# Performance work log

Measured on AMD Instinct MI355X. Metric: run time of the kernel, lower is better.

Reference implementation:

```python
import jax, jax.numpy as jnp
import numpy as np
import math

KEY_SIZE = 128  # init arg; scale = 1/sqrt(key_size)


def setup_inputs() -> dict:
    key = jax.random.key(0)
    kq, kk, kv = jax.random.split(key, 3)
    B, LQ, LK, D, DV = 16, 2048, 2048, 128, 128
    q = jax.random.normal(kq, (B, LQ, D), dtype=jnp.float32)
    k = jax.random.normal(kk, (B, LK, D), dtype=jnp.float32)
    v = jax.random.normal(kv, (B, LK, DV), dtype=jnp.float32)
    return {"q": q, "k": k, "v": v}


def reference(q, k, v):
    scale = 1.0 / math.sqrt(KEY_SIZE)
    # scores: [B, Lq, Lk]
    scores = jnp.einsum('bqd,bkd->bqk', q, k) * scale
    probs = jax.nn.softmax(scores, axis=-1)
    # dropout with p=0.0 is identity (eval-equivalent)
    return jnp.einsum('bqk,bkv->bqv', probs, v)
```

## Files before the change

### kernel.cpp

```cpp
#include <hip/hip_runtime.h>
#include <hip/hip_bf16.h>

typedef float f32x4 __attribute__((ext_vector_type(4)));
typedef float f32x16 __attribute__((ext_vector_type(16)));
typedef short bf16x8 __attribute__((ext_vector_type(8)));
typedef unsigned u32x4 __attribute__((ext_vector_type(4)));

constexpr int NB = 16, LQ = 2048, LK = 2048, D = 128, DV = 128;
constexpr int NTH = 32;
constexpr float SCALE = 0.08838834764831843f;
constexpr float LOG2E = 1.4426950408889634f;
constexpr float QSCALE = SCALE * LOG2E;
constexpr float SHIFT = 12.0f;

__device__ __forceinline__ unsigned short f2bfs(float f) {
  __hip_bfloat16 h = __float2bfloat16(f);
  return __builtin_bit_cast(unsigned short, h);
}

__device__ __forceinline__ unsigned short f2bf(float f) {
  unsigned int u = __float_as_uint(f);
  u += 0x7FFFu + ((u >> 16) & 1u);
  return (unsigned short)(u >> 16);
}

__device__ __forceinline__ int swz2(int row) {
  return (row ^ (row >> 1) ^ (row >> 3)) & 7;
}

__device__ __forceinline__ int swap23(int m) {
  return (m & ~12) | ((m & 4) << 1) | ((m & 8) >> 1);
}

typedef const __attribute__((address_space(1))) void* gas1_t;
typedef __attribute__((address_space(3))) void* las3_t;
__device__ __forceinline__ void gload16(const void* g, void* l) {
  __builtin_amdgcn_global_load_lds((gas1_t)g, (las3_t)l, 16, 0, 0);
}

__device__ __forceinline__ unsigned pk2(float lo, float hi) {
  unsigned short a = f2bfs(lo), b = f2bfs(hi);
  return (unsigned)a | ((unsigned)b << 16);
}

__device__ __forceinline__ void mk_pb(const f32x16& s, bf16x8& pe, bf16x8& po) {
  u32x4 e = {pk2(s[0], s[1]), pk2(s[2], s[3]), pk2(s[4], s[5]), pk2(s[6], s[7])};
  pe = __builtin_bit_cast(bf16x8, e);
  u32x4 od = {pk2(s[8], s[9]), pk2(s[10], s[11]), pk2(s[12], s[13]), pk2(s[14], s[15])};
  po = __builtin_bit_cast(bf16x8, od);
}

__global__ __launch_bounds__(256) void conv_k2(const float* __restrict__ kp,
                                               unsigned short* __restrict__ out) {
  __shared__ __align__(16) unsigned short tk[4096];
  const int T = blockIdx.x, b = blockIdx.y;
  const int tid = threadIdx.x;
  const int k = tid >> 3, cc = tid & 7, d0 = cc * 16;
  const float* src = kp + ((long)(b * LK) + 32 * T + k) * D + d0;
  f32x4 a0 = ((const f32x4*)src)[0];
  f32x4 a1 = ((const f32x4*)src)[1];
  f32x4 a2 = ((const f32x4*)src)[2];
  f32x4 a3 = ((const f32x4*)src)[3];
  bf16x8 r0, r1;
  #pragma unroll
  for (int j = 0; j < 4; ++j) {
    r0[j] = (short)f2bfs(a0[j]); r0[4 + j] = (short)f2bfs(a1[j]);
    r1[j] = (short)f2bfs(a2[j]); r1[4 + j] = (short)f2bfs(a3[j]);
  }
  const int rr = swap23(k);
  *(bf16x8*)&tk[(2 * cc) * 256 + rr * 8] = r0;
  *(bf16x8*)&tk[(2 * cc + 1) * 256 + rr * 8] = r1;
  __syncthreads();
  unsigned short* dst = out + ((long)(b * 64 + T)) * 4096 + tid * 16;
  *(bf16x8*)dst = *(const bf16x8*)&tk[tid * 16];
  *(bf16x8*)(dst + 8) = *(const bf16x8*)&tk[tid * 16 + 8];
}

__global__ __launch_bounds__(256) void conv_v2(const float* __restrict__ vp,
                                               unsigned short* __restrict__ out) {
  __shared__ __align__(16) unsigned short tv[4096];
  const int T = blockIdx.x, b = blockIdx.y;
  const int tid = threadIdx.x;
  const int k = tid >> 3, cc = tid & 7, d0 = cc * 16;
  const float* src = vp + ((long)(b * LK) + 32 * T + k) * DV + d0;
  f32x4 a0 = ((const f32x4*)src)[0];
  f32x4 a1 = ((const f32x4*)src)[1];
  f32x4 a2 = ((const f32x4*)src)[2];
  f32x4 a3 = ((const f32x4*)src)[3];
  unsigned short vals[16];
  #pragma unroll
  for (int j = 0; j < 4; ++j) {
    vals[j]      = f2bfs(a0[j]);
    vals[4 + j]  = f2bfs(a1[j]);
    vals[8 + j]  = f2bfs(a2[j]);
    vals[12 + j] = f2bfs(a3[j]);
  }
  const int vbase = (k >> 3) * 1024 + (k & 7);
  #pragma unroll
  for (int i = 0; i < 16; ++i)
    tv[vbase + (d0 + i) * 8] = vals[i];
  __syncthreads();
  unsigned short* dst = out + ((long)(b * 64 + T)) * 4096 + tid * 16;
  *(bf16x8*)dst = *(const bf16x8*)&tv[tid * 16];
  *(bf16x8*)(dst + 8) = *(const bf16x8*)&tv[tid * 16 + 8];
}

__global__ __launch_bounds__(256, 2) void attn_fwd8(
    const float* __restrict__ qp, const unsigned short* __restrict__ wsK2,
    const unsigned short* __restrict__ wsV2, float* __restrict__ op) {
  __shared__ __align__(16) unsigned short sm[32768];

  const int tid = threadIdx.x;
  const int wid = tid >> 6;
  const int h2  = wid >> 1;
  const int lane = tid & 63;
  const int q32 = lane & 31;
  const int hi  = lane >> 5;
  const int ht  = tid & 127;

  const int bid = blockIdx.x;
  const int sbid = (bid & 7) * 64 + (bid >> 3);
  const int b = sbid >> 5;
  const int qb = (sbid & 31) * 64;
  const int qwave = qb + (wid & 1) * 32;

  bf16x8 aq[8];
  {
    const float* qrow = qp + ((long)(b * LQ + qwave + q32)) * D + hi * 8;
    #pragma unroll
    for (int st = 0; st < 8; ++st) {
      f32x4 x0 = *(const f32x4*)(qrow + st * 16);
      f32x4 x1 = *(const f32x4*)(qrow + st * 16 + 4);
      #pragma unroll
      for (int j = 0; j < 4; ++j) {
        aq[st][j]     = (short)f2bfs(x0[j] * QSCALE);
        aq[st][4 + j] = (short)f2bfs(x1[j] * QSCALE);
      }
    }
  }
  __builtin_amdgcn_sched_barrier(0);

  const int lbase = h2 * 16384;
  const unsigned short* kps = wsK2 + ((long)(b * 64 + h2 * 32)) * 4096;
  const unsigned short* vps = wsV2 + ((long)(b * 64 + h2 * 32)) * 4096;

  auto stage = [&](int buf, int t) {
    const long toff = (long)t * 4096;
    const int lb = lbase + buf * 8192;
    #pragma unroll
    for (int it = 0; it < 4; ++it) {
      const int ci = it * 128 + ht;
      gload16(kps + toff + ci * 8, &sm[lb + ci * 8]);
    }
    #pragma unroll
    for (int it = 0; it < 4; ++it) {
      const int ci = it * 128 + ht;
      gload16(vps + toff + ci * 8, &sm[lb + 4096 + ci * 8]);
    }
  };

  stage(0, 0);
  stage(1, 1);

  f32x16 o[4];
  #pragma unroll
  for (int mt = 0; mt < 4; ++mt) o[mt] = (f32x16){};
  float l_s = 0.f;

  const int kub = lbase + hi * 256 + q32 * 8;
  const int vub = lbase + 4096 + hi * 1024 + q32 * 8;

  for (int t = 0; t < NTH; ++t) {
    if (t < NTH - 1) {
      asm volatile("s_waitcnt vmcnt(8)" ::: "memory");
    } else {
      asm volatile("s_waitcnt vmcnt(0)" ::: "memory");
    }
    __builtin_amdgcn_sched_barrier(0);
    __builtin_amdgcn_s_barrier();
    __builtin_amdgcn_sched_barrier(0);

    const int cur = t & 1;
    const int kb = kub + cur * 8192;
    const int vb = vub + cur * 8192;

    f32x16 s0;
    #pragma unroll
    for (int i = 0; i < 16; ++i) s0[i] = -SHIFT;
    __builtin_amdgcn_s_setprio(1);
    #pragma unroll
    for (int st = 0; st < 8; ++st) {
      bf16x8 k0 = *(const bf16x8*)&sm[kb + st * 512];
      s0 = __builtin_amdgcn_mfma_f32_32x32x16_bf16(k0, aq[st], s0, 0, 0, 0);
    }
    __builtin_amdgcn_s_setprio(0);

    bf16x8 vf[8];
    #pragma unroll
    for (int ks = 0; ks < 2; ++ks)
      #pragma unroll
      for (int mt = 0; mt < 4; ++mt)
        vf[ks * 4 + mt] = *(const bf16x8*)&sm[vb + ks * 2048 + mt * 256];

    #pragma unroll
    for (int i = 0; i < 16; ++i) s0[i] = exp2f(s0[i]);
    float s8[8];
    #pragma unroll
    for (int i = 0; i < 8; ++i) s8[i] = s0[i] + s0[i + 8];
    float s4a = (s8[0] + s8[1]) + (s8[2] + s8[3]);
    float s4b = (s8[4] + s8[5]) + (s8[6] + s8[7]);
    float sum = s4a + s4b;
    l_s += sum + __shfl_xor(sum, 32);

    bf16x8 pb0, pb1;
    mk_pb(s0, pb0, pb1);

    __builtin_amdgcn_s_setprio(1);
    #pragma unroll
    for (int mt = 0; mt < 4; ++mt)
      o[mt] = __builtin_amdgcn_mfma_f32_32x32x16_bf16(vf[mt], pb0, o[mt], 0, 0, 0);
    #pragma unroll
    for (int mt = 0; mt < 4; ++mt)
      o[mt] = __builtin_amdgcn_mfma_f32_32x32x16_bf16(vf[4 + mt], pb1, o[mt], 0, 0, 0);
    __builtin_amdgcn_s_setprio(0);

    __builtin_amdgcn_sched_barrier(0);
    __builtin_amdgcn_s_barrier();
    __builtin_amdgcn_sched_barrier(0);

    if (t < NTH - 2) stage(cur, t + 2);
  }

  float* scr = (float*)sm;
  float* wreg = scr + (size_t)(wid & 1) * 4352;
  __syncthreads();
  if (h2 == 1) {
    #pragma unroll
    for (int j4 = 0; j4 < 16; ++j4) {
      const int mt = j4 >> 2, a = j4 & 3;
      f32x4 v = {o[mt][4 * a], o[mt][4 * a + 1], o[mt][4 * a + 2], o[mt][4 * a + 3]};
      *(f32x4*)&wreg[lane * 64 + ((j4 ^ (lane & 15)) << 2)] = v;
    }
    wreg[4096 + lane] = l_s;
  }
  __syncthreads();
  if (h2 == 0) {
    const float l1 = wreg[4096 + lane];
    const float inv = 1.f / (l_s + l1);
    float* dst = op + ((long)(b * LQ + qwave + q32)) * DV;
    #pragma unroll
    for (int j4 = 0; j4 < 16; ++j4) {
      const int mt = j4 >> 2, a = j4 & 3;
      f32x4 pv = *(const f32x4*)&wreg[lane * 64 + ((j4 ^ (lane & 15)) << 2)];
      f32x4 r;
      #pragma unroll
      for (int i = 0; i < 4; ++i) r[i] = (o[mt][4 * a + i] + pv[i]) * inv;
      *(f32x4*)&dst[32 * mt + 8 * a + 4 * hi] = r;
    }
  }
}

__device__ __forceinline__ int swzc(int row, int c16) {
  return c16 ^ ((row ^ (row >> 3)) & 7);
}

__global__ __launch_bounds__(256, 2) void attn_fwd(
    const float* __restrict__ qp, const float* __restrict__ kp,
    const float* __restrict__ vp, float* __restrict__ op) {
  __shared__ __align__(16) unsigned short smm[28672];
  const int tid = threadIdx.x, wid = tid >> 6, lane = tid & 63;
  const int g = lane >> 4, c = lane & 15;
  const int b = blockIdx.y, qb = blockIdx.x * 64;
  const float* qg = qp + ((long)b * LQ + qb) * D;
  const float* kg = kp + (long)b * LK * D;
  const float* vg = vp + (long)b * LK * DV;
  #pragma unroll
  for (int it = 0; it < 4; ++it) {
    int ch = it * 256 + tid, row = ch >> 4, c16 = ch & 15;
    const float* src = qg + row * D + c16 * 8;
    f32x4 f0 = *(const f32x4*)(src);
    f32x4 f1 = *(const f32x4*)(src + 4);
    bf16x8 fr;
    #pragma unroll
    for (int j = 0; j < 4; ++j) {
      fr[j] = (short)f2bf(f0[j] * SCALE);
      fr[4 + j] = (short)f2bf(f1[j] * SCALE);
    }
    *(bf16x8*)&smm[row * 128 + swzc(row, c16) * 8] = fr;
  }
  __syncthreads();
  bf16x8 aq[4];
  #pragma unroll
  for (int ks = 0; ks < 4; ++ks) {
    int row = wid * 16 + c;
    aq[ks] = *(const bf16x8*)&smm[row * 128 + swzc(row, ks * 4 + g) * 8];
  }
  f32x4 o[8]; f32x4 fz = {0.f, 0.f, 0.f, 0.f};
  #pragma unroll
  for (int i = 0; i < 8; ++i) o[i] = fz;
  float m_r[4] = {-1e30f, -1e30f, -1e30f, -1e30f};
  float l_r[4] = {0.f, 0.f, 0.f, 0.f};
  const int pbase = 24576 + wid * 1024;
  for (int kv0 = 0; kv0 < LK; kv0 += 64) {
    __syncthreads();
    const float* ksrc = kg + (long)kv0 * D;
    #pragma unroll
    for (int it = 0; it < 4; ++it) {
      int ch = it * 256 + tid, row = ch >> 4, c16 = ch & 15;
      const float* src = ksrc + row * D + c16 * 8;
      f32x4 f0 = *(const f32x4*)(src);
      f32x4 f1 = *(const f32x4*)(src + 4);
      bf16x8 fr;
      #pragma unroll
      for (int j = 0; j < 4; ++j) { fr[j] = (short)f2bf(f0[j]); fr[4 + j] = (short)f2bf(f1[j]); }
      *(bf16x8*)&smm[8192 + row * 128 + swzc(row, c16) * 8] = fr;
    }
    {
      const float* vsrc = vg + (long)kv0 * DV;
      int dvq = (tid & 31) * 4, kg8 = tid >> 5;
      f32x4 col[8];
      #pragma unroll
      for (int j = 0; j < 8; ++j) col[j] = *(const f32x4*)(vsrc + (kg8 * 8 + j) * DV + dvq);
      #pragma unroll
      for (int i = 0; i < 4; ++i) {
        int dv = dvq + i;
        bf16x8 fr;
        #pragma unroll
        for (int j = 0; j < 8; ++j) fr[j] = (short)f2bf(col[j][i]);
        *(bf16x8*)&smm[16384 + dv * 64 + swzc(dv, kg8) * 8] = fr;
      }
    }
    __syncthreads();
    f32x4 s[4];
    #pragma unroll
    for (int i = 0; i < 4; ++i) s[i] = fz;
    #pragma unroll
    for (int ks = 0; ks < 4; ++ks) {
      #pragma unroll
      for (int t = 0; t < 4; ++t) {
        int row = t * 16 + c;
        bf16x8 bk = *(const bf16x8*)&smm[8192 + row * 128 + swzc(row, ks * 4 + g) * 8];
        s[t] = __builtin_amdgcn_mfma_f32_16x16x32_bf16(aq[ks], bk, s[t], 0, 0, 0);
      }
    }
    #pragma unroll
    for (int r = 0; r < 4; ++r) {
      float pm = fmaxf(fmaxf(s[0][r], s[1][r]), fmaxf(s[2][r], s[3][r]));
      pm = fmaxf(pm, __shfl_xor(pm, 1));
      pm = fmaxf(pm, __shfl_xor(pm, 2));
      pm = fmaxf(pm, __shfl_xor(pm, 4));
      pm = fmaxf(pm, __shfl_xor(pm, 8));
      float mn = fmaxf(m_r[r], pm);
      float al = exp2f((m_r[r] - mn) * LOG2E);
      float sum = 0.f;
      #pragma unroll
      for (int t = 0; t < 4; ++t) {
        float p = exp2f((s[t][r] - mn) * LOG2E);
        s[t][r] = p; sum += p;
      }
      sum += __shfl_xor(sum, 1); sum += __shfl_xor(sum, 2);
      sum += __shfl_xor(sum, 4); sum += __shfl_xor(sum, 8);
      l_r[r] = l_r[r] * al + sum; m_r[r] = mn;
      #pragma unroll
      for (int dvt = 0; dvt < 8; ++dvt) o[dvt][r] *= al;
    }
    #pragma unroll
    for (int t = 0; t < 4; ++t)
      #pragma unroll
      for (int r = 0; r < 4; ++r) {
        int row = g * 4 + r, colx = c + 16 * t;
        smm[pbase + row * 64 + swzc(row, colx >> 3) * 8 + (colx & 7)] = f2bf(s[t][r]);
      }
    #pragma unroll
    for (int ks = 0; ks < 2; ++ks) {
      bf16x8 pa = *(const bf16x8*)&smm[pbase + c * 64 + swzc(c, ks * 4 + g) * 8];
      #pragma unroll
      for (int dvt = 0; dvt < 8; ++dvt) {
        int row = dvt * 16 + c;
        bf16x8 vb2 = *(const bf16x8*)&smm[16384 + row * 64 + swzc(row, ks * 4 + g) * 8];
        o[dvt] = __builtin_amdgcn_mfma_f32_16x16x32_bf16(pa, vb2, o[dvt], 0, 0, 0);
      }
    }
  }
  float* dst = op + ((long)b * LQ + qb + wid * 16) * DV;
  #pragma unroll
  for (int r = 0; r < 4; ++r) {
    float inv = 1.f / l_r[r];
    #pragma unroll
    for (int dvt = 0; dvt < 8; ++dvt)
      dst[(g * 4 + r) * DV + dvt * 16 + c] = o[dvt][r] * inv;
  }
}

extern "C" void kernel_launch(void* const* d_in, const int* in_sizes, int n_in,
                              void* d_out, int out_size, void* d_ws, size_t ws_size,
                              hipStream_t stream) {
  const float* q = (const float*)d_in[0];
  const float* k = (const float*)d_in[1];
  const float* v = (const float*)d_in[2];
  float* out = (float*)d_out;

  const size_t kelems = (size_t)NB * LK * D;
  const size_t need = kelems * 2 * 2;
  if (ws_size >= need) {
    unsigned short* wsK2 = (unsigned short*)d_ws;
    unsigned short* wsV2 = wsK2 + kelems;
    conv_k2<<<dim3(LK / 32, NB), dim3(256), 0, stream>>>(k, wsK2);
    conv_v2<<<dim3(LK / 32, NB), dim3(256), 0, stream>>>(v, wsV2);
    attn_fwd8<<<dim3(NB * LQ / 64), dim3(256), 0, stream>>>(q, wsK2, wsV2, out);
  } else {
    attn_fwd<<<dim3(LQ / 64, NB), dim3(256), 0, stream>>>(q, k, v, out);
  }
}
```

Measured before the change: 74.25 us.

## Software-pipeline QK scores one tile ahead of the softmax and PV stage

Restructures the attention main loop so that each iteration computes the QK^T MFMAs for tile t while doing exp2, row-sum and PV MFMAs on the scores of tile t-1. V fragments are prefetched into registers at the end of each iteration, and a prologue and epilogue handle the first and last tiles. The intent is to hide the exp/convert latency behind independent matrix-core work and to free the LDS buffer earlier for staging. In exchange, more values stay live in VGPRs (two score tiles plus the V fragments), which could cause spills or limit occupancy.

```diff
diff --git a/kernel.cpp b/kernel.cpp
--- a/kernel.cpp
+++ b/kernel.cpp
@@ -105,7 +105,7 @@
   *(bf16x8*)(dst + 8) = *(const bf16x8*)&tv[tid * 16 + 8];
 }
 
-__global__ __launch_bounds__(256, 2) void attn_fwd8(
+__global__ __launch_bounds__(256, 2) void attn_fwd9(
     const float* __restrict__ qp, const unsigned short* __restrict__ wsK2,
     const unsigned short* __restrict__ wsV2, float* __restrict__ op) {
   __shared__ __align__(16) unsigned short sm[32768];
@@ -170,7 +170,33 @@
   const int kub = lbase + hi * 256 + q32 * 8;
   const int vub = lbase + 4096 + hi * 1024 + q32 * 8;
 
-  for (int t = 0; t < NTH; ++t) {
+  asm volatile("s_waitcnt vmcnt(8)" ::: "memory");
+  __builtin_amdgcn_sched_barrier(0);
+  __builtin_amdgcn_s_barrier();
+  __builtin_amdgcn_sched_barrier(0);
+
+  f32x16 s_cur;
+  #pragma unroll
+  for (int i = 0; i < 16; ++i) s_cur[i] = -SHIFT;
+  #pragma unroll
+  for (int st = 0; st < 8; ++st) {
+    bf16x8 k0 = *(const bf16x8*)&sm[kub + st * 512];
+    s_cur = __builtin_amdgcn_mfma_f32_32x32x16_bf16(k0, aq[st], s_cur, 0, 0, 0);
+  }
+  bf16x8 vf[8];
+  #pragma unroll
+  for (int ks = 0; ks < 2; ++ks)
+    #pragma unroll
+    for (int mt = 0; mt < 4; ++mt)
+      vf[ks * 4 + mt] = *(const bf16x8*)&sm[vub + ks * 2048 + mt * 256];
+
+  asm volatile("s_waitcnt lgkmcnt(0)" ::: "memory");
+  __builtin_amdgcn_sched_barrier(0);
+  __builtin_amdgcn_s_barrier();
+  __builtin_amdgcn_sched_barrier(0);
+  stage(0, 2);
+
+  for (int t = 1; t < NTH; ++t) {
     if (t < NTH - 1) {
       asm volatile("s_waitcnt vmcnt(8)" ::: "memory");
     } else {
@@ -184,36 +210,27 @@
     const int kb = kub + cur * 8192;
     const int vb = vub + cur * 8192;
 
-    f32x16 s0;
-    #pragma unroll
-    for (int i = 0; i < 16; ++i) s0[i] = -SHIFT;
+    f32x16 s_new;
+    #pragma unroll
+    for (int i = 0; i < 16; ++i) s_new[i] = -SHIFT;
     __builtin_amdgcn_s_setprio(1);
     #pragma unroll
     for (int st = 0; st < 8; ++st) {
       bf16x8 k0 = *(const bf16x8*)&sm[kb + st * 512];
-      s0 = __builtin_amdgcn_mfma_f32_32x32x16_bf16(k0, aq[st], s0, 0, 0, 0);
+      s_new = __builtin_amdgcn_mfma_f32_32x32x16_bf16(k0, aq[st], s_new, 0, 0, 0);
     }
     __builtin_amdgcn_s_setprio(0);
 
-    bf16x8 vf[8];
-    #pragma unroll
-    for (int ks = 0; ks < 2; ++ks)
-      #pragma unroll
-      for (int mt = 0; mt < 4; ++mt)
-        vf[ks * 4 + mt] = *(const bf16x8*)&sm[vb + ks * 2048 + mt * 256];
-
-    #pragma unroll
-    for (int i = 0; i < 16; ++i) s0[i] = exp2f(s0[i]);
+    #pragma unroll
+    for (int i = 0; i < 16; ++i) s_cur[i] = exp2f(s_cur[i]);
     float s8[8];
     #pragma unroll
-    for (int i = 0; i < 8; ++i) s8[i] = s0[i] + s0[i + 8];
-    float s4a = (s8[0] + s8[1]) + (s8[2] + s8[3]);
-    float s4b = (s8[4] + s8[5]) + (s8[6] + s8[7]);
-    float sum = s4a + s4b;
+    for (int i = 0; i < 8; ++i) s8[i] = s_cur[i] + s_cur[i + 8];
+    float sum = ((s8[0] + s8[1]) + (s8[2] + s8[3])) +
+                ((s8[4] + s8[5]) + (s8[6] + s8[7]));
     l_s += sum + __shfl_xor(sum, 32);
-
     bf16x8 pb0, pb1;
-    mk_pb(s0, pb0, pb1);
+    mk_pb(s_cur, pb0, pb1);
 
     __builtin_amdgcn_s_setprio(1);
     #pragma unroll
@@ -224,11 +241,38 @@
       o[mt] = __builtin_amdgcn_mfma_f32_32x32x16_bf16(vf[4 + mt], pb1, o[mt], 0, 0, 0);
     __builtin_amdgcn_s_setprio(0);
 
+    #pragma unroll
+    for (int ks = 0; ks < 2; ++ks)
+      #pragma unroll
+      for (int mt = 0; mt < 4; ++mt)
+        vf[ks * 4 + mt] = *(const bf16x8*)&sm[vb + ks * 2048 + mt * 256];
+
+    asm volatile("s_waitcnt lgkmcnt(0)" ::: "memory");
     __builtin_amdgcn_sched_barrier(0);
     __builtin_amdgcn_s_barrier();
     __builtin_amdgcn_sched_barrier(0);
-
-    if (t < NTH - 2) stage(cur, t + 2);
+    if (t + 2 < NTH) stage(cur, t + 2);
+
+    s_cur = s_new;
+  }
+
+  {
+    #pragma unroll
+    for (int i = 0; i < 16; ++i) s_cur[i] = exp2f(s_cur[i]);
+    float s8[8];
+    #pragma unroll
+    for (int i = 0; i < 8; ++i) s8[i] = s_cur[i] + s_cur[i + 8];
+    float sum = ((s8[0] + s8[1]) + (s8[2] + s8[3])) +
+                ((s8[4] + s8[5]) + (s8[6] + s8[7]));
+    l_s += sum + __shfl_xor(sum, 32);
+    bf16x8 pb0, pb1;
+    mk_pb(s_cur, pb0, pb1);
+    #pragma unroll
+    for (int mt = 0; mt < 4; ++mt)
+      o[mt] = __builtin_amdgcn_mfma_f32_32x32x16_bf16(vf[mt], pb0, o[mt], 0, 0, 0);
+    #pragma unroll
+    for (int mt = 0; mt < 4; ++mt)
+      o[mt] = __builtin_amdgcn_mfma_f32_32x32x16_bf16(vf[4 + mt], pb1, o[mt], 0, 0, 0);
   }
 
   float* scr = (float*)sm;
@@ -407,7 +451,7 @@
     unsigned short* wsV2 = wsK2 + kelems;
     conv_k2<<<dim3(LK / 32, NB), dim3(256), 0, stream>>>(k, wsK2);
     conv_v2<<<dim3(LK / 32, NB), dim3(256), 0, stream>>>(v, wsV2);
-    attn_fwd8<<<dim3(NB * LQ / 64), dim3(256), 0, stream>>>(q, wsK2, wsV2, out);
+    attn_fwd9<<<dim3(NB * LQ / 64), dim3(256), 0, stream>>>(q, wsK2, wsV2, out);
   } else {
     attn_fwd<<<dim3(LQ / 64, NB), dim3(256), 0, stream>>>(q, k, v, out);
   }
```

After: 75.93 us. 2.3% more time.
